# Optimization experiments

Hardware: AMD Instinct MI355X
Metric: run time of the kernel (lower is better)

## Reference

```python
import jax, jax.numpy as jnp
import numpy as np

NUM_BASES = 8


def setup_inputs() -> dict:
    key = jax.random.key(0)
    ks = jax.random.split(key, 8)
    N, E = 100000, 1600000
    IN_F, OUT_F, NUM_RELS = 128, 128, 16
    si = IN_F // NUM_BASES   # 16
    so = OUT_F // NUM_BASES  # 16
    return {
        "h": jax.random.normal(ks[0], (N, IN_F), dtype=jnp.float32),
        "norm": jax.random.uniform(ks[1], (N, 1), dtype=jnp.float32),
        "edge_src": jax.random.randint(ks[2], (E,), 0, N, dtype=jnp.int32),
        "edge_dst": jax.random.randint(ks[3], (E,), 0, N, dtype=jnp.int32),
        "edge_type": jax.random.randint(ks[4], (E,), 0, NUM_RELS, dtype=jnp.int32),
        "weight": jax.random.normal(ks[5], (NUM_RELS, NUM_BASES * si * so), dtype=jnp.float32) * 0.1,
        "bias_param": jax.random.normal(ks[6], (OUT_F,), dtype=jnp.float32) * 0.1,
        "loop_weight": jax.random.normal(ks[7], (IN_F, OUT_F), dtype=jnp.float32) * 0.1,
    }


def reference(h, norm, edge_src, edge_dst, edge_type, weight, bias_param, loop_weight):
    N, in_feat = h.shape
    out_feat = loop_weight.shape[1]
    si = in_feat // NUM_BASES
    so = out_feat // NUM_BASES
    E = edge_type.shape[0]

    # self-loop message (dropout=0.0 -> identity)
    loop_message = h @ loop_weight                      # [N, out_feat]

    # msg_func: gather per-edge relation weight blocks and do block-diag bmm
    W = weight[edge_type].reshape(E, NUM_BASES, si, so)  # [E, B, si, so]
    src = h[edge_src].reshape(E, NUM_BASES, si)          # [E, B, si]
    msg = jnp.einsum("ebi,ebio->ebo", src, W).reshape(E, out_feat)

    # scatter-sum messages to destination nodes, rescale by norm
    agg = jax.ops.segment_sum(msg, edge_dst, num_segments=N)  # [N, out_feat]
    node_repr = agg * norm

    # bias + self-loop + activation
    node_repr = node_repr + bias_param + loop_message
    return jax.nn.relu(node_repr)
```

## Files before the change

kernel.cpp:

```cpp
#include <hip/hip_runtime.h>


typedef float nfloat4 __attribute__((ext_vector_type(4)));

__device__ __forceinline__ unsigned int f2bf(float f) {
  const unsigned int u = __float_as_uint(f);
  return (u + 0x7FFFu + ((u >> 16) & 1u)) >> 16;
}

__global__ __launch_bounds__(256) void rgcn_loopm_kernel(
    const float* __restrict__ h, const float* __restrict__ loop_w,
    const float* __restrict__ bias, unsigned int* __restrict__ loopm, int N) {
  __shared__ float lw[128 * 128];
  for (int idx = threadIdx.x; idx < 128 * 128 / 4; idx += 256) {
    ((float4*)lw)[idx] = ((const float4*)loop_w)[idx];
  }
  __syncthreads();

  const int lane = threadIdx.x & 63;
  const int wid = threadIdx.x >> 6;
  const int group0 = blockIdx.x * 4 + wid;
  const int ngroups = gridDim.x * 4;
  const int totgroups = (N + 3) >> 2;
  const float b0 = bias[lane];
  const float b1 = bias[64 + lane];

  for (int g = group0; g < totgroups; g += ngroups) {
    const int n0 = g * 4;
    const int nn = (N - n0 < 4) ? (N - n0) : 4;
    if (nn == 4) {
      const float* __restrict__ r0 = h + (size_t)n0 * 128;
      const float* __restrict__ r1 = r0 + 128;
      const float* __restrict__ r2 = r1 + 128;
      const float* __restrict__ r3 = r2 + 128;
      float a00 = b0, a01 = b1, a10 = b0, a11 = b1;
      float a20 = b0, a21 = b1, a30 = b0, a31 = b1;
#pragma unroll 4
      for (int k = 0; k < 128; ++k) {
        const float w0 = lw[k * 128 + lane];
        const float w1 = lw[k * 128 + 64 + lane];
        a00 = fmaf(r0[k], w0, a00); a01 = fmaf(r0[k], w1, a01);
        a10 = fmaf(r1[k], w0, a10); a11 = fmaf(r1[k], w1, a11);
        a20 = fmaf(r2[k], w0, a20); a21 = fmaf(r2[k], w1, a21);
        a30 = fmaf(r3[k], w0, a30); a31 = fmaf(r3[k], w1, a31);
      }
      loopm[(size_t)(n0 + 0) * 64 + lane] = f2bf(a00) | (f2bf(a01) << 16);
      loopm[(size_t)(n0 + 1) * 64 + lane] = f2bf(a10) | (f2bf(a11) << 16);
      loopm[(size_t)(n0 + 2) * 64 + lane] = f2bf(a20) | (f2bf(a21) << 16);
      loopm[(size_t)(n0 + 3) * 64 + lane] = f2bf(a30) | (f2bf(a31) << 16);
    } else {
      for (int r = 0; r < nn; ++r) {
        const int n = n0 + r;
        const float* __restrict__ hr = h + (size_t)n * 128;
        float a0 = b0, a1 = b1;
#pragma unroll 4
        for (int k = 0; k < 128; ++k) {
          const float a = hr[k];
          a0 = fmaf(a, lw[k * 128 + lane], a0);
          a1 = fmaf(a, lw[k * 128 + 64 + lane], a1);
        }
        loopm[(size_t)n * 64 + lane] = f2bf(a0) | (f2bf(a1) << 16);
      }
    }
  }
}

__global__ __launch_bounds__(256) void rgcn_init_kernel(
    const float* __restrict__ h, const float* __restrict__ loop_w,
    const float* __restrict__ bias, float* __restrict__ out, int N) {
  __shared__ float lw[128 * 128];
  for (int idx = threadIdx.x; idx < 128 * 128 / 4; idx += 256) {
    ((float4*)lw)[idx] = ((const float4*)loop_w)[idx];
  }
  __syncthreads();
  const int lane = threadIdx.x & 63;
  const int wid = threadIdx.x >> 6;
  const int group0 = blockIdx.x * 4 + wid;
  const int ngroups = gridDim.x * 4;
  const float b0 = bias[lane];
  const float b1 = bias[64 + lane];
  for (int g = group0; g < (N + 3) >> 2; g += ngroups) {
    const int n0 = g * 4;
    const int nn = (N - n0 < 4) ? (N - n0) : 4;
    for (int r = 0; r < nn; ++r) {
      const int n = n0 + r;
      const float* __restrict__ hr = h + (size_t)n * 128;
      float a0 = b0, a1 = b1;
#pragma unroll 4
      for (int k = 0; k < 128; ++k) {
        const float a = hr[k];
        a0 = fmaf(a, lw[k * 128 + lane], a0);
        a1 = fmaf(a, lw[k * 128 + 64 + lane], a1);
      }
      out[(size_t)n * 128 + lane] = a0;
      out[(size_t)n * 128 + 64 + lane] = a1;
    }
  }
}

__global__ __launch_bounds__(1024) void rgcn_precompute_kernel(
    const float* __restrict__ h, const float* __restrict__ weight,
    unsigned int* __restrict__ M, int base, int cend) {
  __shared__ unsigned int st[4 * 1024];
  const int tid = threadIdx.x;
  const int lane = tid & 63;
  const int t = tid >> 6;
  const int b = lane >> 4;
  const int o = lane & 15;

  const float* __restrict__ wb = weight + t * 2048 + b * 256 + o;
  float wlo[16], whi[16];
#pragma unroll
  for (int i = 0; i < 16; ++i) {
    wlo[i] = wb[i * 16];
    whi[i] = wb[1024 + i * 16];
  }

  const int span = cend - base;
  const int ngroups = (span + 3) >> 2;

  for (int g = blockIdx.x; g < ngroups; g += gridDim.x) {
    const int n0 = base + g * 4;
#pragma unroll
    for (int j = 0; j < 4; ++j) {
      const int n = n0 + j;
      unsigned int pk = 0;
      if (n < cend) {
        const float4* __restrict__ hp =
            (const float4*)(h + (size_t)n * 128) + (b << 2);
        const float4 x0 = hp[0], x1 = hp[1], x2 = hp[2], x3 = hp[3];
        const float4 y0 = hp[16], y1 = hp[17], y2 = hp[18], y3 = hp[19];

        float a0 = x0.x * wlo[0], a1 = x0.y * wlo[1];
        a0 = fmaf(x0.z, wlo[2], a0);  a1 = fmaf(x0.w, wlo[3], a1);
        a0 = fmaf(x1.x, wlo[4], a0);  a1 = fmaf(x1.y, wlo[5], a1);
        a0 = fmaf(x1.z, wlo[6], a0);  a1 = fmaf(x1.w, wlo[7], a1);
        a0 = fmaf(x2.x, wlo[8], a0);  a1 = fmaf(x2.y, wlo[9], a1);
        a0 = fmaf(x2.z, wlo[10], a0); a1 = fmaf(x2.w, wlo[11], a1);
        a0 = fmaf(x3.x, wlo[12], a0); a1 = fmaf(x3.y, wlo[13], a1);
        a0 = fmaf(x3.z, wlo[14], a0); a1 = fmaf(x3.w, wlo[15], a1);

        float c0 = y0.x * whi[0], c1 = y0.y * whi[1];
        c0 = fmaf(y0.z, whi[2], c0);  c1 = fmaf(y0.w, whi[3], c1);
        c0 = fmaf(y1.x, whi[4], c0);  c1 = fmaf(y1.y, whi[5], c1);
        c0 = fmaf(y1.z, whi[6], c0);  c1 = fmaf(y1.w, whi[7], c1);
        c0 = fmaf(y2.x, whi[8], c0);  c1 = fmaf(y2.y, whi[9], c1);
        c0 = fmaf(y2.z, whi[10], c0); c1 = fmaf(y2.w, whi[11], c1);
        c0 = fmaf(y3.x, whi[12], c0); c1 = fmaf(y3.y, whi[13], c1);
        c0 = fmaf(y3.z, whi[14], c0); c1 = fmaf(y3.w, whi[15], c1);

        pk = f2bf(a0 + a1) | (f2bf(c0 + c1) << 16);
      }
      st[j * 1024 + tid] = pk;
    }
    __syncthreads();

    const size_t dst = ((size_t)(n0 - base)) << 10;
    if (n0 + 4 <= cend) {
      const nfloat4 v = ((const nfloat4*)st)[tid];
      __builtin_nontemporal_store(v, ((nfloat4*)(M + dst)) + tid);
    } else {
      const int valid = (cend - n0) << 10;
      for (int k = tid; k < valid; k += 1024) M[dst + k] = st[k];
    }
    __syncthreads();
  }
}

__global__ __launch_bounds__(256) void rgcn_zero_kernel(int* __restrict__ p,
                                                        int n) {
  for (int i = blockIdx.x * 256 + threadIdx.x; i < n; i += gridDim.x * 256)
    p[i] = 0;
}

__global__ __launch_bounds__(256) void rgcn_hist_kernel(
    const int* __restrict__ esrc, const int* __restrict__ edst,
    int* __restrict__ cnt, int E, int N, unsigned S) {
  for (int e = blockIdx.x * 256 + threadIdx.x; e < E; e += gridDim.x * 256) {
    const unsigned q = (unsigned)esrc[e] / S;
    atomicAdd(&cnt[(int)(q * (unsigned)N) + edst[e]], 1);
  }
}

__global__ __launch_bounds__(1024) void rgcn_scan_pass1(
    const int* __restrict__ cnt, int* __restrict__ partial, int bins) {
  __shared__ int sums[1024];
  const int t = threadIdx.x;
  const int base = blockIdx.x * 4096 + t * 4;
  int s = 0;
  if (base + 3 < bins) {
    const int4 v = *(const int4*)(cnt + base);
    s = v.x + v.y + v.z + v.w;
  } else {
    for (int j = 0; j < 4; ++j)
      if (base + j < bins) s += cnt[base + j];
  }
  sums[t] = s;
  __syncthreads();
  for (int off = 512; off > 0; off >>= 1) {
    if (t < off) sums[t] += sums[t + off];
    __syncthreads();
  }
  if (t == 0) partial[blockIdx.x] = sums[0];
}

__global__ __launch_bounds__(1024) void rgcn_scan_pass2(
    int* __restrict__ partial, int nb) {
  __shared__ int sc[1024];
  const int t = threadIdx.x;
  int v[4];
  int s = 0;
#pragma unroll
  for (int j = 0; j < 4; ++j) {
    const int i = t * 4 + j;
    v[j] = (i < nb) ? partial[i] : 0;
    s += v[j];
  }
  sc[t] = s;
  __syncthreads();
#pragma unroll
  for (int off = 1; off < 1024; off <<= 1) {
    const int add = (t >= off) ? sc[t - off] : 0;
    __syncthreads();
    sc[t] += add;
    __syncthreads();
  }
  int run = (t == 0) ? 0 : sc[t - 1];
#pragma unroll
  for (int j = 0; j < 4; ++j) {
    const int i = t * 4 + j;
    if (i < nb) partial[i] = run;
    run += v[j];
  }
}

__global__ __launch_bounds__(1024) void rgcn_scan_pass3(
    const int* __restrict__ cnt, const int* __restrict__ partial,
    int* __restrict__ row_ptr, int* __restrict__ cursor, int bins) {
  __shared__ int sums[1024];
  const int t = threadIdx.x;
  const int base = blockIdx.x * 4096 + t * 4;
  int v0 = 0, v1 = 0, v2 = 0, v3 = 0;
  if (base + 3 < bins) {
    const int4 v = *(const int4*)(cnt + base);
    v0 = v.x; v1 = v.y; v2 = v.z; v3 = v.w;
  } else {
    if (base < bins) v0 = cnt[base];
    if (base + 1 < bins) v1 = cnt[base + 1];
    if (base + 2 < bins) v2 = cnt[base + 2];
  }
  sums[t] = v0 + v1 + v2 + v3;
  __syncthreads();
#pragma unroll
  for (int off = 1; off < 1024; off <<= 1) {
    const int add = (t >= off) ? sums[t - off] : 0;
    __syncthreads();
    sums[t] += add;
    __syncthreads();
  }
  const int run = partial[blockIdx.x] + ((t == 0) ? 0 : sums[t - 1]);
  const int p0 = run, p1 = p0 + v0, p2 = p1 + v1, p3 = p2 + v2;
  if (base + 3 < bins) {
    *(int4*)(row_ptr + base) = make_int4(p0, p1, p2, p3);
    *(int4*)(cursor + base) = make_int4(p0, p1, p2, p3);
  } else {
    if (base < bins) { row_ptr[base] = p0; cursor[base] = p0; }
    if (base + 1 < bins) { row_ptr[base + 1] = p1; cursor[base + 1] = p1; }
    if (base + 2 < bins) { row_ptr[base + 2] = p2; cursor[base + 2] = p2; }
  }
}

__global__ void rgcn_set_kernel(int* __restrict__ p, int v) {
  if (threadIdx.x == 0) *p = v;
}

__global__ __launch_bounds__(256) void rgcn_scatter_kernel(
    const int* __restrict__ esrc, const int* __restrict__ edst,
    const int* __restrict__ etype, int* __restrict__ cursor,
    int* __restrict__ srec, int E, int N, unsigned S) {
  for (int e = blockIdx.x * 256 + threadIdx.x; e < E; e += gridDim.x * 256) {
    const unsigned s = (unsigned)esrc[e];
    const unsigned q = s / S;
    const int key = (int)(q * (unsigned)N) + edst[e];
    const int p = atomicAdd(&cursor[key], 1);
    srec[p] = (int)((s - q * S) << 4) | etype[e];
  }
}

__global__ __launch_bounds__(256) void rgcn_gather3_kernel(
    const float* __restrict__ norm, const int* __restrict__ srec,
    const int* __restrict__ rpc, const unsigned int* __restrict__ M,
    const unsigned int* __restrict__ loopm, float* __restrict__ out, int N,
    int mode) {
  const int lane = threadIdx.x & 63;
  const int w0 = blockIdx.x * 4 + (threadIdx.x >> 6);
  const int nw = gridDim.x * 4;
  const bool first = (mode & 1) != 0;
  const bool final_pass = (mode & 2) != 0;

  for (int d = w0; d < N; d += nw) {
    const int e0 = rpc[d];
    const int e1 = rpc[d + 1];
    if (!first && !final_pass && e0 == e1) continue;

    float acc0 = 0.f, acc1 = 0.f;
    int e = e0;
    for (; e + 8 <= e1; e += 8) {
      const int r0 = srec[e], r1 = srec[e + 1], r2 = srec[e + 2],
                r3 = srec[e + 3], r4 = srec[e + 4], r5 = srec[e + 5],
                r6 = srec[e + 6], r7 = srec[e + 7];
      const unsigned int v0 = __builtin_nontemporal_load(&M[(size_t)r0 * 64 + lane]);
      const unsigned int v1 = __builtin_nontemporal_load(&M[(size_t)r1 * 64 + lane]);
      const unsigned int v2 = __builtin_nontemporal_load(&M[(size_t)r2 * 64 + lane]);
      const unsigned int v3 = __builtin_nontemporal_load(&M[(size_t)r3 * 64 + lane]);
      const unsigned int v4 = __builtin_nontemporal_load(&M[(size_t)r4 * 64 + lane]);
      const unsigned int v5 = __builtin_nontemporal_load(&M[(size_t)r5 * 64 + lane]);
      const unsigned int v6 = __builtin_nontemporal_load(&M[(size_t)r6 * 64 + lane]);
      const unsigned int v7 = __builtin_nontemporal_load(&M[(size_t)r7 * 64 + lane]);
      acc0 += __uint_as_float(v0 << 16);
      acc1 += __uint_as_float(v0 & 0xFFFF0000u);
      acc0 += __uint_as_float(v1 << 16);
      acc1 += __uint_as_float(v1 & 0xFFFF0000u);
      acc0 += __uint_as_float(v2 << 16);
      acc1 += __uint_as_float(v2 & 0xFFFF0000u);
      acc0 += __uint_as_float(v3 << 16);
      acc1 += __uint_as_float(v3 & 0xFFFF0000u);
      acc0 += __uint_as_float(v4 << 16);
      acc1 += __uint_as_float(v4 & 0xFFFF0000u);
      acc0 += __uint_as_float(v5 << 16);
      acc1 += __uint_as_float(v5 & 0xFFFF0000u);
      acc0 += __uint_as_float(v6 << 16);
      acc1 += __uint_as_float(v6 & 0xFFFF0000u);
      acc0 += __uint_as_float(v7 << 16);
      acc1 += __uint_as_float(v7 & 0xFFFF0000u);
    }
    for (; e < e1; ++e) {
      const unsigned int v = __builtin_nontemporal_load(&M[(size_t)srec[e] * 64 + lane]);
      acc0 += __uint_as_float(v << 16);
      acc1 += __uint_as_float(v & 0xFFFF0000u);
    }

    float* __restrict__ op = out + ((size_t)d << 7);
    if (!first) {
      acc0 += op[lane];
      acc1 += op[64 + lane];
    }
    if (final_pass) {
      const float nm = norm[d];
      const unsigned int lp = loopm[(size_t)d * 64 + lane];
      op[lane] = fmaxf(fmaf(acc0, nm, __uint_as_float(lp << 16)), 0.f);
      op[64 + lane] =
          fmaxf(fmaf(acc1, nm, __uint_as_float(lp & 0xFFFF0000u)), 0.f);
    } else {
      op[lane] = acc0;
      op[64 + lane] = acc1;
    }
  }
}

__global__ __launch_bounds__(256) void rgcn_edge_kernel(
    const float* __restrict__ h, const float* __restrict__ norm,
    const int* __restrict__ esrc, const int* __restrict__ edst,
    const int* __restrict__ etype, const float* __restrict__ weight,
    float* __restrict__ out, int E) {
  const int lane = threadIdx.x & 63;
  const int wid = threadIdx.x >> 6;
  const int wave0 = blockIdx.x * 4 + wid;
  const int nwaves = gridDim.x * 4;
  const int b = lane >> 4;
  const int o = lane & 15;

  for (int e = wave0; e < E; e += nwaves) {
    const int src = esrc[e];
    const int dst = edst[e];
    const int et = etype[e];
    const float s_lo = h[src * 128 + lane];
    const float s_hi = h[src * 128 + 64 + lane];
    const float nrm = norm[dst];
    const float* __restrict__ Wb = weight + et * 2048 + b * 256 + o;
    float m0 = 0.f, m1 = 0.f;
#pragma unroll
    for (int i = 0; i < 16; ++i) {
      const float a_lo = __shfl(s_lo, (lane & 48) + i, 64);
      const float a_hi = __shfl(s_hi, (lane & 48) + i, 64);
      m0 = fmaf(a_lo, Wb[i * 16], m0);
      m1 = fmaf(a_hi, Wb[1024 + i * 16], m1);
    }
    atomicAdd(&out[dst * 128 + lane], m0 * nrm);
    atomicAdd(&out[dst * 128 + 64 + lane], m1 * nrm);
  }
}

__global__ __launch_bounds__(256) void rgcn_relu_kernel(float* __restrict__ out,
                                                        int total4) {
  int i = blockIdx.x * 256 + threadIdx.x;
  const int stride = gridDim.x * 256;
  for (; i < total4; i += stride) {
    float4 v = ((float4*)out)[i];
    v.x = fmaxf(v.x, 0.f);
    v.y = fmaxf(v.y, 0.f);
    v.z = fmaxf(v.z, 0.f);
    v.w = fmaxf(v.w, 0.f);
    ((float4*)out)[i] = v;
  }
}

extern "C" void kernel_launch(void* const* d_in, const int* in_sizes, int n_in,
                              void* d_out, int out_size, void* d_ws, size_t ws_size,
                              hipStream_t stream) {
  const float* h      = (const float*)d_in[0];
  const float* norm   = (const float*)d_in[1];
  const int*   esrc   = (const int*)d_in[2];
  const int*   edst   = (const int*)d_in[3];
  const int*   etype  = (const int*)d_in[4];
  const float* weight = (const float*)d_in[5];
  const float* bias   = (const float*)d_in[6];
  const float* loop_w = (const float*)d_in[7];
  float* out = (float*)d_out;

  const int N = in_sizes[0] / 128;
  const int E = in_sizes[2];
  const int nrels = in_sizes[5] / 2048;

  int C = -1, S = 0;
  size_t ofs_rp = 0, ofs_cur = 0, ofs_part = 0, ofs_srec = 0, ofs_lpm = 0,
         ofs_M = 0;
  if (nrels == 16 && N >= 1 && N < (1 << 26)) {
    for (int cc = 1; cc <= 64; ++cc) {
      const size_t bins = (size_t)cc * (size_t)N;
      if (bins > (size_t)4096 * 4096) break;
      const int ss = (N + cc - 1) / cc;
      const size_t o_rp = (bins + 3) & ~(size_t)3;
      const size_t o_cur = (o_rp + bins + 1 + 3) & ~(size_t)3;
      const size_t o_part = (o_cur + bins + 3) & ~(size_t)3;
      const size_t o_srec = o_part + 4096;
      const size_t o_lpm = (o_srec + (size_t)E + 15) & ~(size_t)15;
      const size_t o_M = o_lpm + (size_t)N * 64;
      const size_t need = (o_M + (size_t)ss * 16 * 64) * 4;
      if (need <= ws_size) {
        C = cc; S = ss;
        ofs_rp = o_rp; ofs_cur = o_cur; ofs_part = o_part;
        ofs_srec = o_srec; ofs_lpm = o_lpm; ofs_M = o_M;
        break;
      }
    }
  }

  if (C >= 1) {
    const int bins = C * N;
    const int nb = (bins + 4095) / 4096;
    int* base    = (int*)d_ws;
    int* cnt     = base;
    int* row_ptr = base + ofs_rp;
    int* cursor  = base + ofs_cur;
    int* partial = base + ofs_part;
    int* srec    = base + ofs_srec;
    unsigned int* loopm = (unsigned int*)(base + ofs_lpm);
    unsigned int* M     = (unsigned int*)(base + ofs_M);

    rgcn_loopm_kernel<<<2048, 256, 0, stream>>>(h, loop_w, bias, loopm, N);
    rgcn_zero_kernel<<<1024, 256, 0, stream>>>(cnt, bins);
    rgcn_hist_kernel<<<2048, 256, 0, stream>>>(esrc, edst, cnt, E, N,
                                               (unsigned)S);
    rgcn_scan_pass1<<<nb, 1024, 0, stream>>>(cnt, partial, bins);
    rgcn_scan_pass2<<<1, 1024, 0, stream>>>(partial, nb);
    rgcn_scan_pass3<<<nb, 1024, 0, stream>>>(cnt, partial, row_ptr, cursor,
                                             bins);
    rgcn_set_kernel<<<1, 64, 0, stream>>>(row_ptr + bins, E);
    rgcn_scatter_kernel<<<2048, 256, 0, stream>>>(esrc, edst, etype, cursor,
                                                  srec, E, N, (unsigned)S);
    for (int c = 0; c < C; ++c) {
      const int cbase = c * S;
      const int cend = (cbase + S < N) ? (cbase + S) : N;
      if (cbase >= N) break;
      rgcn_precompute_kernel<<<512, 1024, 0, stream>>>(h, weight, M, cbase,
                                                       cend);
      const int mode = (c == 0 ? 1 : 0) | (c == C - 1 ? 2 : 0);
      rgcn_gather3_kernel<<<2048, 256, 0, stream>>>(
          norm, srec, row_ptr + (size_t)c * N, M, loopm, out, N, mode);
    }
  } else {
    rgcn_init_kernel<<<2048, 256, 0, stream>>>(h, loop_w, bias, out, N);
    rgcn_edge_kernel<<<4096, 256, 0, stream>>>(h, norm, esrc, edst, etype,
                                               weight, out, E);
    rgcn_relu_kernel<<<2048, 256, 0, stream>>>(out, (N * 128) / 4);
  }
}
```

Before: 912.9 us.

## Store inter-chunk partial sums as packed bf16 in workspace buffer

Between source chunks, the per-node running sums now go to a separate workspace buffer as packed bf16 pairs instead of fp32 rows in the output. This halves the bytes read and written for partials on every chunk pass. The gather loads of M switch from nontemporal to normal cached loads, the skip for nodes with no edges is removed, and the gather grid doubles. Rounding partials to bf16 after each chunk adds accumulated precision error, and the workspace now needs N*64 more words when there is more than one chunk, which may change how many chunks are chosen.

Measured after the change: 939.8 us. 1.03x slower.

```diff
diff --git a/kernel.cpp b/kernel.cpp
--- a/kernel.cpp
+++ b/kernel.cpp
@@ -290,8 +290,8 @@
 __global__ __launch_bounds__(256) void rgcn_gather3_kernel(
     const float* __restrict__ norm, const int* __restrict__ srec,
     const int* __restrict__ rpc, const unsigned int* __restrict__ M,
-    const unsigned int* __restrict__ loopm, float* __restrict__ out, int N,
-    int mode) {
+    const unsigned int* __restrict__ loopm, unsigned int* __restrict__ part,
+    float* __restrict__ out, int N, int mode) {
   const int lane = threadIdx.x & 63;
   const int w0 = blockIdx.x * 4 + (threadIdx.x >> 6);
   const int nw = gridDim.x * 4;
@@ -301,7 +301,6 @@
   for (int d = w0; d < N; d += nw) {
     const int e0 = rpc[d];
     const int e1 = rpc[d + 1];
-    if (!first && !final_pass && e0 == e1) continue;
 
     float acc0 = 0.f, acc1 = 0.f;
     int e = e0;
@@ -309,14 +308,14 @@
       const int r0 = srec[e], r1 = srec[e + 1], r2 = srec[e + 2],
                 r3 = srec[e + 3], r4 = srec[e + 4], r5 = srec[e + 5],
                 r6 = srec[e + 6], r7 = srec[e + 7];
-      const unsigned int v0 = __builtin_nontemporal_load(&M[(size_t)r0 * 64 + lane]);
-      const unsigned int v1 = __builtin_nontemporal_load(&M[(size_t)r1 * 64 + lane]);
-      const unsigned int v2 = __builtin_nontemporal_load(&M[(size_t)r2 * 64 + lane]);
-      const unsigned int v3 = __builtin_nontemporal_load(&M[(size_t)r3 * 64 + lane]);
-      const unsigned int v4 = __builtin_nontemporal_load(&M[(size_t)r4 * 64 + lane]);
-      const unsigned int v5 = __builtin_nontemporal_load(&M[(size_t)r5 * 64 + lane]);
-      const unsigned int v6 = __builtin_nontemporal_load(&M[(size_t)r6 * 64 + lane]);
-      const unsigned int v7 = __builtin_nontemporal_load(&M[(size_t)r7 * 64 + lane]);
+      const unsigned int v0 = M[(size_t)r0 * 64 + lane];
+      const unsigned int v1 = M[(size_t)r1 * 64 + lane];
+      const unsigned int v2 = M[(size_t)r2 * 64 + lane];
+      const unsigned int v3 = M[(size_t)r3 * 64 + lane];
+      const unsigned int v4 = M[(size_t)r4 * 64 + lane];
+      const unsigned int v5 = M[(size_t)r5 * 64 + lane];
+      const unsigned int v6 = M[(size_t)r6 * 64 + lane];
+      const unsigned int v7 = M[(size_t)r7 * 64 + lane];
       acc0 += __uint_as_float(v0 << 16);
       acc1 += __uint_as_float(v0 & 0xFFFF0000u);
       acc0 += __uint_as_float(v1 << 16);
@@ -335,25 +334,25 @@
       acc1 += __uint_as_float(v7 & 0xFFFF0000u);
     }
     for (; e < e1; ++e) {
-      const unsigned int v = __builtin_nontemporal_load(&M[(size_t)srec[e] * 64 + lane]);
+      const unsigned int v = M[(size_t)srec[e] * 64 + lane];
       acc0 += __uint_as_float(v << 16);
       acc1 += __uint_as_float(v & 0xFFFF0000u);
     }
 
-    float* __restrict__ op = out + ((size_t)d << 7);
     if (!first) {
-      acc0 += op[lane];
-      acc1 += op[64 + lane];
+      const unsigned int pp = part[(size_t)d * 64 + lane];
+      acc0 += __uint_as_float(pp << 16);
+      acc1 += __uint_as_float(pp & 0xFFFF0000u);
     }
     if (final_pass) {
       const float nm = norm[d];
       const unsigned int lp = loopm[(size_t)d * 64 + lane];
+      float* __restrict__ op = out + ((size_t)d << 7);
       op[lane] = fmaxf(fmaf(acc0, nm, __uint_as_float(lp << 16)), 0.f);
       op[64 + lane] =
           fmaxf(fmaf(acc1, nm, __uint_as_float(lp & 0xFFFF0000u)), 0.f);
     } else {
-      op[lane] = acc0;
-      op[64 + lane] = acc1;
+      part[(size_t)d * 64 + lane] = f2bf(acc0) | (f2bf(acc1) << 16);
     }
   }
 }
@@ -424,7 +423,7 @@
 
   int C = -1, S = 0;
   size_t ofs_rp = 0, ofs_cur = 0, ofs_part = 0, ofs_srec = 0, ofs_lpm = 0,
-         ofs_M = 0;
+         ofs_pb = 0, ofs_M = 0;
   if (nrels == 16 && N >= 1 && N < (1 << 26)) {
     for (int cc = 1; cc <= 64; ++cc) {
       const size_t bins = (size_t)cc * (size_t)N;
@@ -435,12 +434,13 @@
       const size_t o_part = (o_cur + bins + 3) & ~(size_t)3;
       const size_t o_srec = o_part + 4096;
       const size_t o_lpm = (o_srec + (size_t)E + 15) & ~(size_t)15;
-      const size_t o_M = o_lpm + (size_t)N * 64;
+      const size_t o_pb = o_lpm + (size_t)N * 64;
+      const size_t o_M = o_pb + ((cc > 1) ? (size_t)N * 64 : 0);
       const size_t need = (o_M + (size_t)ss * 16 * 64) * 4;
       if (need <= ws_size) {
         C = cc; S = ss;
         ofs_rp = o_rp; ofs_cur = o_cur; ofs_part = o_part;
-        ofs_srec = o_srec; ofs_lpm = o_lpm; ofs_M = o_M;
+        ofs_srec = o_srec; ofs_lpm = o_lpm; ofs_pb = o_pb; ofs_M = o_M;
         break;
       }
     }
@@ -456,6 +456,7 @@
     int* partial = base + ofs_part;
     int* srec    = base + ofs_srec;
     unsigned int* loopm = (unsigned int*)(base + ofs_lpm);
+    unsigned int* partb = (unsigned int*)(base + ofs_pb);
     unsigned int* M     = (unsigned int*)(base + ofs_M);
 
     rgcn_loopm_kernel<<<2048, 256, 0, stream>>>(h, loop_w, bias, loopm, N);
@@ -476,8 +477,8 @@
       rgcn_precompute_kernel<<<512, 1024, 0, stream>>>(h, weight, M, cbase,
                                                        cend);
       const int mode = (c == 0 ? 1 : 0) | (c == C - 1 ? 2 : 0);
-      rgcn_gather3_kernel<<<2048, 256, 0, stream>>>(
-          norm, srec, row_ptr + (size_t)c * N, M, loopm, out, N, mode);
+      rgcn_gather3_kernel<<<4096, 256, 0, stream>>>(
+          norm, srec, row_ptr + (size_t)c * N, M, loopm, partb, out, N, mode);
     }
   } else {
     rgcn_init_kernel<<<2048, 256, 0, stream>>>(h, loop_w, bias, out, N);
```
